# Optimization experiments

Measured on AMD Instinct MI355X. Metric: run time of the kernel, lower is better.

The kernel has to match this reference:

```python
import jax, jax.numpy as jnp
import numpy as np

VOCAB, ATTR, B = 50257, 16, 256
EMB, ATTR_EMB, HID, ZDIM = 300, 200, 700, 500
MAXLEN = 30
SOS_IDX, EOS_IDX = 1, 2


def setup_inputs() -> dict:
    ks = jax.random.split(jax.random.key(0), 8)
    s = 0.02
    return {
        "z": jax.random.normal(ks[0], (B, ZDIM), jnp.float32),
        "l": jax.random.randint(ks[1], (B,), 0, ATTR),
        "emb_w": jax.random.normal(ks[2], (VOCAB, EMB), jnp.float32) * s,
        "attr_w": jax.random.normal(ks[3], (ATTR, ATTR_EMB), jnp.float32) * s,
        "W_ih": jax.random.normal(ks[4], (3 * HID, EMB), jnp.float32) * s,
        "W_hh": jax.random.normal(ks[5], (3 * HID, HID), jnp.float32) * s,
        "b_ih": jnp.zeros((3 * HID,), jnp.float32),
        "b_hh": jnp.zeros((3 * HID,), jnp.float32),
        "out_w": jax.random.normal(ks[6], (VOCAB, HID), jnp.float32) * s,
        "out_b": jnp.zeros((VOCAB,), jnp.float32),
    }


def gru_cell(x, h, W_ih, W_hh, b_ih, b_hh):
    # PyTorch GRU cell: r,z,n gate ordering
    gi = x @ W_ih.T + b_ih          # (B, 3H)
    gh = h @ W_hh.T + b_hh          # (B, 3H)
    i_r, i_z, i_n = jnp.split(gi, 3, axis=-1)
    h_r, h_z, h_n = jnp.split(gh, 3, axis=-1)
    r = jax.nn.sigmoid(i_r + h_r)
    zg = jax.nn.sigmoid(i_z + h_z)
    n = jnp.tanh(i_n + r * h_n)
    return (1.0 - zg) * n + zg * h


def reference(z, l, emb_w, attr_w, W_ih, W_hh, b_ih, b_hh, out_w, out_b):
    # hidden init: cat([z (B,500), attr_emb(l) (B,200)]) -> (B,700)
    h0 = jnp.concatenate([z, attr_w[l]], axis=-1)
    tok0 = jnp.full((B,), SOS_IDX, jnp.int32)
    keys = jax.random.split(jax.random.key(42), MAXLEN)

    def step(carry, k):
        h, tok = carry
        x = emb_w[tok]                                   # (B,300)
        h = gru_cell(x, h, W_ih, W_hh, b_ih, b_hh)       # (B,700)
        logits = h @ out_w.T + out_b                     # (B,VOCAB)
        # multinomial(softmax(logits), 1).detach()
        nxt = jax.lax.stop_gradient(
            jax.random.categorical(k, logits).astype(jnp.int32))
        return (h, nxt), (h, nxt)

    (h_last, _), (hy_t, y_t) = jax.lax.scan(step, (h0, tok0), keys)
    # final forced-EOS step
    eos = jnp.full((B,), EOS_IDX, jnp.int32)
    h_final = gru_cell(emb_w[eos], h_last, W_ih, W_hh, b_ih, b_hh)
    hy = jnp.concatenate([jnp.transpose(hy_t, (1, 0, 2)), h_final[:, None, :]], axis=1)  # (B,MAXLEN+1,700)
    y = jnp.concatenate([jnp.transpose(y_t, (1, 0)), eos[:, None]], axis=1)              # (B,MAXLEN+1)
    return hy, y
```

## Files before the change

### kernel.cpp

```cpp
#include <hip/hip_runtime.h>
#include <stdint.h>

#define VOCAB 50257
#define B 256
#define EMB 300
#define HID 700
#define G3 2100
#define ZDIM 500
#define ATTR_EMBD 200
#define MAXLEN 30
#define SEQ 31
#define HY_ELEMS (B*SEQ*HID)
#define KP 704
#define NKT 22
#define KIH 320
#define VPAD 50304
#define NVT 393
#define MPAD 2112
#define SOS_IDX 1
#define EOS_IDX 2
#define CHUNK 4096
#define TILE_STRIDE ((size_t)NKT * 2 * CHUNK)
#define NIT5 1572
#define NBLK5 1576

typedef _Float16 half8 __attribute__((ext_vector_type(8)));
typedef _Float16 half4 __attribute__((ext_vector_type(4)));
typedef float f32x4 __attribute__((ext_vector_type(4)));

typedef const __attribute__((address_space(1))) void* gas1_t;
typedef __attribute__((address_space(3))) void* las3_t;
__device__ __forceinline__ void gload_lds16(const void* g, void* l) {
  __builtin_amdgcn_global_load_lds((gas1_t)g, (las3_t)l, 16, 0, 0);
}

__device__ __forceinline__ uint32_t rotl32(uint32_t x, int r) {
  return (x << r) | (x >> (32 - r));
}

__device__ __forceinline__ void threefry2x32(uint32_t k0, uint32_t k1,
                                             uint32_t x0, uint32_t x1,
                                             uint32_t& o0, uint32_t& o1) {
  const uint32_t ks2 = k0 ^ k1 ^ 0x1BD11BDAu;
  x0 += k0; x1 += k1;
#define TF_R4(a, b, c, d)                                     \
  x0 += x1; x1 = rotl32(x1, a); x1 ^= x0;                     \
  x0 += x1; x1 = rotl32(x1, b); x1 ^= x0;                     \
  x0 += x1; x1 = rotl32(x1, c); x1 ^= x0;                     \
  x0 += x1; x1 = rotl32(x1, d); x1 ^= x0;
  TF_R4(13, 15, 26, 6)  x0 += k1;  x1 += ks2 + 1u;
  TF_R4(17, 29, 16, 24) x0 += ks2; x1 += k0 + 2u;
  TF_R4(13, 15, 26, 6)  x0 += k0;  x1 += k1 + 3u;
  TF_R4(17, 29, 16, 24) x0 += k1;  x1 += ks2 + 4u;
  TF_R4(13, 15, 26, 6)  x0 += ks2; x1 += k0 + 5u;
#undef TF_R4
  o0 = x0; o1 = x1;
}

__device__ __forceinline__ unsigned long long gumbel_pack(float s, uint32_t key0,
                                                          uint32_t key1, int b, int v) {
  uint32_t j = (uint32_t)(b * VOCAB + v);
  uint32_t o0, o1;
  threefry2x32(key0, key1, 0u, j, o0, o1);
  uint32_t bits = o0 ^ o1;
  float f = __uint_as_float((bits >> 9) | 0x3f800000u) - 1.0f;
  float u = fmaxf(f, 1.17549435e-38f);
  float g = -__logf(-__logf(u));
  s += g;
  uint32_t us = __float_as_uint(s);
  us = (us & 0x80000000u) ? ~us : (us | 0x80000000u);
  return ((unsigned long long)us << 32) | (uint32_t)(~(uint32_t)v);
}

struct hl16 { _Float16 hi, lo; };
__device__ __forceinline__ hl16 split16(float val, float scale) {
  float s = val * scale;
  _Float16 h = (_Float16)s;
  hl16 r;
  r.hi = h;
  r.lo = (_Float16)(s - (float)h);
  return r;
}

__global__ void k_init(const float* __restrict__ z, const int* __restrict__ l,
                       const float* __restrict__ attr_w, const float* __restrict__ emb_w,
                       float* __restrict__ hbuf0, uint32_t* __restrict__ keys,
                       unsigned long long* __restrict__ slots,
                       int* __restrict__ tok, float* __restrict__ y_out,
                       _Float16* __restrict__ h_hi, _Float16* __restrict__ h_lo,
                       _Float16* __restrict__ ht,
                       _Float16* __restrict__ x0_hi, _Float16* __restrict__ x0_lo,
                       _Float16* __restrict__ xe_hi, _Float16* __restrict__ xe_lo,
                       int full) {
  int idx = blockIdx.x * blockDim.x + threadIdx.x;
  if (idx < B * HID) {
    int b = idx / HID, i = idx % HID;
    float v = (i < ZDIM) ? z[b * ZDIM + i]
                         : attr_w[l[b] * ATTR_EMBD + (i - ZDIM)];
    hbuf0[idx] = v;
    hl16 r = split16(v, 8.0f);
    h_hi[b * KP + i] = r.hi;
    h_lo[b * KP + i] = r.lo;
  }
  if (idx < MAXLEN) {
    uint32_t o0, o1;
    threefry2x32(0u, 42u, 0u, (uint32_t)idx, o0, o1);
    keys[2 * idx] = o0; keys[2 * idx + 1] = o1;
  }
  if (idx < MAXLEN * B) slots[idx] = 0ull;
  if (idx < B) {
    tok[idx] = SOS_IDX;
    tok[31 * B + idx] = EOS_IDX;
    y_out[idx * SEQ + MAXLEN] = 2.0f;
  }
  if (idx < B * 4) {
    int b = idx >> 2, k = HID + (idx & 3);
    h_hi[b * KP + k] = (_Float16)0.0f;
    h_lo[b * KP + k] = (_Float16)0.0f;
    int c = b >> 7, row = b & 127, e = k & 7;
    size_t tb = (size_t)c * TILE_STRIDE + (size_t)21 * 2 * CHUNK
              + (3 * 128 + row) * 8 + e;
    ht[tb] = (_Float16)0.0f;
    ht[tb + CHUNK] = (_Float16)0.0f;
  }
  if (full && idx < KIH) {
    float v0 = (idx < EMB) ? emb_w[SOS_IDX * EMB + idx] : 0.0f;
    float ve = (idx < EMB) ? emb_w[EOS_IDX * EMB + idx] : 0.0f;
    hl16 r0 = split16(v0, 8.0f);
    hl16 re = split16(ve, 8.0f);
    for (int b = 0; b < B; ++b) {
      x0_hi[b * KIH + idx] = r0.hi; x0_lo[b * KIH + idx] = r0.lo;
      xe_hi[b * KIH + idx] = re.hi; xe_lo[b * KIH + idx] = re.lo;
    }
  }
}

__global__ void k_wsplit(const float* __restrict__ out_w, _Float16* __restrict__ wt) {
  size_t idx = (size_t)blockIdx.x * blockDim.x + threadIdx.x;
  if (idx >= (size_t)NVT * NKT * 1024) return;
  int h4 = (int)(idx & 1023);
  int ktp = (int)(idx >> 10);
  int kt = ktp % NKT, p = ktp / NKT;
  int slot4 = h4 >> 1, e0 = (h4 & 1) * 4;
  int kc = slot4 >> 7, row = slot4 & 127;
  int v = p * 128 + row;
  int k = kt * 32 + kc * 8 + e0;
  float x[4];
  if (v < VOCAB && k + 3 < HID) {
    const float4 xv = *(const float4*)&out_w[(size_t)v * HID + k];
    x[0] = xv.x; x[1] = xv.y; x[2] = xv.z; x[3] = xv.w;
  } else {
#pragma unroll
    for (int j = 0; j < 4; ++j)
      x[j] = (v < VOCAB && k + j < HID) ? out_w[(size_t)v * HID + k + j] : 0.0f;
  }
  half4 hi, lo;
#pragma unroll
  for (int j = 0; j < 4; ++j) {
    hl16 r = split16(x[j], 64.0f);
    hi[j] = r.hi; lo[j] = r.lo;
  }
  size_t base = (size_t)p * TILE_STRIDE + (size_t)kt * 2 * CHUNK + slot4 * 8 + e0;
  *(half4*)&wt[base] = hi;
  *(half4*)&wt[base + CHUNK] = lo;
}

__global__ void k_gwsplit(const float* __restrict__ src, _Float16* __restrict__ hi,
                          _Float16* __restrict__ lo, int Msrc, int Ksrc, int Kpad,
                          int tot4) {
  int idx = blockIdx.x * blockDim.x + threadIdx.x;
  if (idx >= tot4) return;
  size_t i4 = (size_t)idx * 4;
  int m = (int)(i4 / Kpad), k = (int)(i4 % Kpad);
  half4 h, l;
#pragma unroll
  for (int j = 0; j < 4; ++j) {
    float x = (m < Msrc && k + j < Ksrc) ? src[(size_t)m * Ksrc + k + j] : 0.0f;
    hl16 r = split16(x, 64.0f);
    h[j] = r.hi; l[j] = r.lo;
  }
  *(half4*)&hi[i4] = h;
  *(half4*)&lo[i4] = l;
}

__global__ __launch_bounds__(256, 4)
void k_gates2(const _Float16* __restrict__ wih_hi, const _Float16* __restrict__ wih_lo,
              const _Float16* __restrict__ whh_hi, const _Float16* __restrict__ whh_lo,
              const _Float16* __restrict__ x_hi, const _Float16* __restrict__ x_lo,
              const _Float16* __restrict__ h_hi, const _Float16* __restrict__ h_lo,
              float* __restrict__ gi, float* __restrict__ gh) {
  const int zz = blockIdx.z;
  const _Float16* __restrict__ Whi = zz ? whh_hi : wih_hi;
  const _Float16* __restrict__ Wlo = zz ? whh_lo : wih_lo;
  const _Float16* __restrict__ Xhi = zz ? h_hi : x_hi;
  const _Float16* __restrict__ Xlo = zz ? h_lo : x_lo;
  const int Kz = zz ? KP : KIH;
  float* __restrict__ out = zz ? gh : gi;

  const int jbase = blockIdx.x * 64;
  const int bbase = blockIdx.y * 64;
  __shared__ float4 lds[2][4][256];
  const int tid = threadIdx.x, lane = tid & 63, wid = tid >> 6;
  const int wj = wid >> 1, wb2 = wid & 1;
  const size_t wrow = (size_t)(jbase + lane) * Kz;
  const size_t xrow = (size_t)(bbase + lane) * Kz;

  f32x4 acc[2][2];
#pragma unroll
  for (int i = 0; i < 2; ++i)
#pragma unroll
    for (int j = 0; j < 2; ++j) acc[i][j] = (f32x4)0.0f;

#define GSTAGE(bf, k0)                                                   \
  {                                                                      \
    gload_lds16(Whi + wrow + (k0) + wid * 8, &lds[bf][0][wid * 64]);     \
    gload_lds16(Wlo + wrow + (k0) + wid * 8, &lds[bf][1][wid * 64]);     \
    gload_lds16(Xhi + xrow + (k0) + wid * 8, &lds[bf][2][wid * 64]);     \
    gload_lds16(Xlo + xrow + (k0) + wid * 8, &lds[bf][3][wid * 64]);     \
  }

  const int nt = Kz / 32;
  GSTAGE(0, 0)
  for (int kt = 0; kt < nt; ++kt) {
    const int cur = kt & 1;
    __syncthreads();
    if (kt + 1 < nt) GSTAGE(cur ^ 1, (kt + 1) * 32)
    const int kcf = (lane >> 4) * 64 + (lane & 15);
    half8 a_hi[2], a_lo[2];
#pragma unroll
    for (int fv = 0; fv < 2; ++fv) {
      int s = kcf + wj * 32 + fv * 16;
      a_hi[fv] = *(const half8*)&lds[cur][0][s];
      a_lo[fv] = *(const half8*)&lds[cur][1][s];
    }
#pragma unroll
    for (int fb = 0; fb < 2; ++fb) {
      int s = kcf + wb2 * 32 + fb * 16;
      half8 b_hi = *(const half8*)&lds[cur][2][s];
      half8 b_lo = *(const half8*)&lds[cur][3][s];
#pragma unroll
      for (int fv = 0; fv < 2; ++fv) {
        acc[fv][fb] = __builtin_amdgcn_mfma_f32_16x16x32_f16(a_hi[fv], b_hi,
                                                             acc[fv][fb], 0, 0, 0);
        acc[fv][fb] = __builtin_amdgcn_mfma_f32_16x16x32_f16(a_hi[fv], b_lo,
                                                             acc[fv][fb], 0, 0, 0);
        acc[fv][fb] = __builtin_amdgcn_mfma_f32_16x16x32_f16(a_lo[fv], b_hi,
                                                             acc[fv][fb], 0, 0, 0);
      }
    }
  }
#undef GSTAGE

  const float c2 = 1.0f / 512.0f;
#pragma unroll
  for (int fb = 0; fb < 2; ++fb) {
    const int b = bbase + wb2 * 32 + fb * 16 + (lane & 15);
#pragma unroll
    for (int fv = 0; fv < 2; ++fv) {
#pragma unroll
      for (int r = 0; r < 4; ++r) {
        int j = jbase + wj * 32 + fv * 16 + (lane >> 4) * 4 + r;
        if (j < G3) out[b * G3 + j] = acc[fv][fb][r] * c2;
      }
    }
  }
}

__global__ void k_gates(const float* __restrict__ W_ih, const float* __restrict__ W_hh,
                        const float* __restrict__ emb_w, const float* __restrict__ hprev,
                        const int* __restrict__ tok,
                        float* __restrict__ gi, float* __restrict__ gh) {
  const int zz = blockIdx.z;
  const float* __restrict__ W = zz ? W_hh : W_ih;
  const int K = zz ? HID : EMB;
  float* __restrict__ out = zz ? gh : gi;
  __shared__ float w_lds[20][36];
  __shared__ float xh_lds[20][36];
  const int jbase = blockIdx.x * 32;
  const int bbase = blockIdx.y * 32;
  const int tid = threadIdx.x;
  const int tj = tid % 16, tb = tid / 16;
  float a00 = 0.f, a01 = 0.f, a10 = 0.f, a11 = 0.f;
  for (int k0 = 0; k0 < K; k0 += 20) {
    for (int idx = tid; idx < 640; idx += 256) {
      int col = idx / 20, kk = idx % 20;
      int j = jbase + col;
      w_lds[kk][col] = (j < G3) ? W[j * K + k0 + kk] : 0.0f;
      int b = bbase + col;
      float xv;
      if (zz) xv = hprev[b * HID + k0 + kk];
      else    xv = emb_w[tok[b] * EMB + k0 + kk];
      xh_lds[kk][col] = xv;
    }
    __syncthreads();
#pragma unroll
    for (int kk = 0; kk < 20; ++kk) {
      float w0 = w_lds[kk][tj * 2], w1 = w_lds[kk][tj * 2 + 1];
      float h0 = xh_lds[kk][tb * 2], h1 = xh_lds[kk][tb * 2 + 1];
      a00 += w0 * h0; a01 += w0 * h1;
      a10 += w1 * h0; a11 += w1 * h1;
    }
    __syncthreads();
  }
  int j0 = jbase + tj * 2, b0 = bbase + tb * 2;
  if (j0 < G3)     { out[b0 * G3 + j0] = a00;     out[(b0 + 1) * G3 + j0] = a01; }
  if (j0 + 1 < G3) { out[b0 * G3 + j0 + 1] = a10; out[(b0 + 1) * G3 + j0 + 1] = a11; }
}

__global__ void k_hnew(const float* __restrict__ gi, const float* __restrict__ gh,
                       const float* __restrict__ b_ih, const float* __restrict__ b_hh,
                       const float* __restrict__ hprev, float* __restrict__ hnext,
                       float* __restrict__ hy, _Float16* __restrict__ h_hi,
                       _Float16* __restrict__ h_lo, _Float16* __restrict__ ht, int t) {
  int idx = blockIdx.x * blockDim.x + threadIdx.x;
  if (idx >= B * HID) return;
  int b = idx / HID, i = idx % HID;
  float ir = gi[b * G3 + i]            + b_ih[i];
  float iz = gi[b * G3 + HID + i]      + b_ih[HID + i];
  float in_ = gi[b * G3 + 2 * HID + i] + b_ih[2 * HID + i];
  float hr = gh[b * G3 + i]            + b_hh[i];
  float hz = gh[b * G3 + HID + i]      + b_hh[HID + i];
  float hn = gh[b * G3 + 2 * HID + i]  + b_hh[2 * HID + i];
  float r  = 1.0f / (1.0f + expf(-(ir + hr)));
  float zg = 1.0f / (1.0f + expf(-(iz + hz)));
  float n  = tanhf(in_ + r * hn);
  float h  = (1.0f - zg) * n + zg * hprev[idx];
  hnext[idx] = h;
  hy[(size_t)b * SEQ * HID + (size_t)t * HID + i] = h;
  hl16 rr = split16(h, 8.0f);
  h_hi[b * KP + i] = rr.hi;
  h_lo[b * KP + i] = rr.lo;
  int c = b >> 7, row = b & 127;
  size_t tb = (size_t)c * TILE_STRIDE + (size_t)(i >> 5) * 2 * CHUNK
            + ((((i >> 3) & 3) * 128 + row) * 8) + (i & 7);
  ht[tb] = rr.hi;
  ht[tb + CHUNK] = rr.lo;
}

__global__ __launch_bounds__(256, 4)
void k_logits5(const _Float16* __restrict__ wt, const _Float16* __restrict__ ht,
               const float* __restrict__ out_b, const uint32_t* __restrict__ keys,
               unsigned long long* __restrict__ slot, int t) {
  const int item = (blockIdx.x & 7) * 197 + (blockIdx.x >> 3);
  if (item >= NIT5) return;
  const int p = item >> 2, vh = (item >> 1) & 1, c = item & 1;

  __shared__ float4 ldsh[2][1024];
  const int tid = threadIdx.x, lane = tid & 63, wid = tid >> 6;
  const int wv = wid >> 1, wb = wid & 1;
  const int lq = lane >> 4, lr = lane & 15;

  const _Float16* __restrict__ wp = wt + (size_t)p * TILE_STRIDE;
  const _Float16* __restrict__ hp = ht + (size_t)c * TILE_STRIDE;

  const int wslot = lq * 128 + vh * 64 + wv * 32 + lr;
  const int hslot = lq * 128 + wb * 64 + lr;

  f32x4 acc[2][4];
#pragma unroll
  for (int i = 0; i < 2; ++i)
#pragma unroll
    for (int j = 0; j < 4; ++j) acc[i][j] = (f32x4)0.0f;

  half8 wA[4], wB[4];

#define LOADW(W, ktv)                                                         \
  {                                                                           \
    const _Float16* bw = wp + (size_t)(ktv) * (2 * CHUNK);                    \
    _Pragma("unroll")                                                         \
    for (int fv = 0; fv < 2; ++fv) {                                          \
      W[fv * 2 + 0] = *(const half8*)(bw + (wslot + fv * 16) * 8);            \
      W[fv * 2 + 1] = *(const half8*)(bw + CHUNK + (wslot + fv * 16) * 8);    \
    }                                                                         \
  }
#define STAGEH(bf, ktv)                                                       \
  {                                                                           \
    const _Float16* bh = hp + (size_t)(ktv) * (2 * CHUNK);                    \
    _Pragma("unroll")                                                         \
    for (int j = 0; j < 4; ++j)                                               \
      gload_lds16(bh + (j * 256 + wid * 64 + lane) * 8,                       \
                  &ldsh[bf][j * 256 + wid * 64]);                             \
  }
#define COMPUTE(bf, W)                                                        \
  _Pragma("unroll")                                                           \
  for (int fb = 0; fb < 4; ++fb) {                                            \
    half8 hhi = *(const half8*)&ldsh[bf][hslot + fb * 16];                    \
    half8 hlo = *(const half8*)&ldsh[bf][512 + hslot + fb * 16];              \
    _Pragma("unroll")                                                         \
    for (int fv = 0; fv < 2; ++fv) {                                          \
      acc[fv][fb] = __builtin_amdgcn_mfma_f32_16x16x32_f16(                   \
          W[fv * 2 + 0], hhi, acc[fv][fb], 0, 0, 0);                          \
      acc[fv][fb] = __builtin_amdgcn_mfma_f32_16x16x32_f16(                   \
          W[fv * 2 + 0], hlo, acc[fv][fb], 0, 0, 0);                          \
      acc[fv][fb] = __builtin_amdgcn_mfma_f32_16x16x32_f16(                   \
          W[fv * 2 + 1], hhi, acc[fv][fb], 0, 0, 0);                          \
    }                                                                         \
  }

  LOADW(wA, 0)
  STAGEH(0, 0)
  __syncthreads();
#pragma unroll 1
  for (int kt = 0; kt < NKT; kt += 2) {
    if (kt + 1 < NKT) { STAGEH(1, kt + 1) LOADW(wB, kt + 1) }
    COMPUTE(0, wA)
    __syncthreads();
    if (kt + 2 < NKT) { STAGEH(0, kt + 2) LOADW(wA, kt + 2) }
    COMPUTE(1, wB)
    __syncthreads();
  }
#undef LOADW
#undef STAGEH
#undef COMPUTE

  const uint32_t key0 = keys[2 * t], key1 = keys[2 * t + 1];
  const float c2 = 1.0f / 512.0f;
  const int vbase0 = p * 128 + vh * 64 + wv * 32;
#pragma unroll
  for (int fb = 0; fb < 4; ++fb) {
    const int b = c * 128 + wb * 64 + fb * 16 + lr;
    unsigned long long best = 0ull;
#pragma unroll
    for (int fv = 0; fv < 2; ++fv) {
#pragma unroll
      for (int r = 0; r < 4; ++r) {
        int v = vbase0 + fv * 16 + lq * 4 + r;
        if (v < VOCAB) {
          float s = acc[fv][fb][r] * c2 + out_b[v];
          unsigned long long cand = gumbel_pack(s, key0, key1, b, v);
          if (cand > best) best = cand;
        }
      }
    }
    unsigned long long o;
    o = __shfl_xor(best, 16, 64); if (o > best) best = o;
    o = __shfl_xor(best, 32, 64); if (o > best) best = o;
    if (lq == 0) atomicMax(&slot[b], best);
  }
}

#define WPITCH 68
#define HPITCH 260
__global__ __launch_bounds__(256)
void k_logits_f32(const float* __restrict__ h, const float* __restrict__ out_w,
                  const float* __restrict__ out_b, const uint32_t* __restrict__ keys,
                  unsigned long long* __restrict__ slot, int t) {
  __shared__ float w_lds[20][WPITCH];
  __shared__ float h_lds[20][HPITCH];
  const int vbase = blockIdx.x * 64;
  const int tid = threadIdx.x;
  const int tv = tid % 8, tb = tid / 8;
  float acc[8][8];
#pragma unroll
  for (int i = 0; i < 8; ++i)
#pragma unroll
    for (int j = 0; j < 8; ++j) acc[i][j] = 0.f;

  for (int k0 = 0; k0 < HID; k0 += 20) {
    for (int idx = tid; idx < 64 * 20; idx += 256) {
      int vv = idx / 20, kk = idx % 20;
      int v = vbase + vv;
      w_lds[kk][vv] = (v < VOCAB) ? out_w[(size_t)v * HID + k0 + kk] : 0.0f;
    }
    for (int idx = tid; idx < 256 * 20; idx += 256) {
      int bb = idx / 20, kk = idx % 20;
      h_lds[kk][bb] = h[bb * HID + k0 + kk];
    }
    __syncthreads();
#pragma unroll
    for (int kk = 0; kk < 20; ++kk) {
      float wv[8], hv[8];
      *(float4*)&wv[0] = *(const float4*)&w_lds[kk][tv * 8];
      *(float4*)&wv[4] = *(const float4*)&w_lds[kk][tv * 8 + 4];
      *(float4*)&hv[0] = *(const float4*)&h_lds[kk][tb * 8];
      *(float4*)&hv[4] = *(const float4*)&h_lds[kk][tb * 8 + 4];
#pragma unroll
      for (int iv = 0; iv < 8; ++iv)
#pragma unroll
        for (int ib = 0; ib < 8; ++ib) acc[iv][ib] += wv[iv] * hv[ib];
    }
    __syncthreads();
  }

  const uint32_t key0 = keys[2 * t], key1 = keys[2 * t + 1];
#pragma unroll
  for (int ib = 0; ib < 8; ++ib) {
    const int b = tb * 8 + ib;
    unsigned long long best = 0ull;
#pragma unroll
    for (int iv = 0; iv < 8; ++iv) {
      int v = vbase + tv * 8 + iv;
      if (v >= VOCAB) continue;
      unsigned long long cand = gumbel_pack(acc[iv][ib] + out_b[v], key0, key1, b, v);
      if (cand > best) best = cand;
    }
#pragma unroll
    for (int off = 1; off < 8; off <<= 1) {
      unsigned long long other = __shfl_xor(best, off, 64);
      if (other > best) best = other;
    }
    if (tv == 0) atomicMax(&slot[b], best);
  }
}

__global__ void k_tok2(const unsigned long long* __restrict__ slot,
                       const float* __restrict__ emb_w,
                       int* __restrict__ tok_next, float* __restrict__ y_out,
                       _Float16* __restrict__ xc_hi, _Float16* __restrict__ xc_lo,
                       int t, int full) {
  const int b = blockIdx.x;
  const int c = threadIdx.x;
  unsigned long long p = slot[b];
  uint32_t v = ~((uint32_t)(p & 0xFFFFFFFFull));
  if (c == 0) {
    tok_next[b] = (int)v;
    y_out[b * SEQ + t] = (float)v;
  }
  if (!full) return;
  if (c < 75) {
    float4 xv = *(const float4*)&emb_w[(size_t)v * EMB + c * 4];
    half4 hi, lo;
    hl16 r0 = split16(xv.x, 8.0f); hi[0] = r0.hi; lo[0] = r0.lo;
    hl16 r1 = split16(xv.y, 8.0f); hi[1] = r1.hi; lo[1] = r1.lo;
    hl16 r2 = split16(xv.z, 8.0f); hi[2] = r2.hi; lo[2] = r2.lo;
    hl16 r3 = split16(xv.w, 8.0f); hi[3] = r3.hi; lo[3] = r3.lo;
    *(half4*)&xc_hi[b * KIH + c * 4] = hi;
    *(half4*)&xc_lo[b * KIH + c * 4] = lo;
  } else if (c < 80) {
    *(half4*)&xc_hi[b * KIH + c * 4] = (half4)(_Float16)0.0f;
    *(half4*)&xc_lo[b * KIH + c * 4] = (half4)(_Float16)0.0f;
  }
}

extern "C" void kernel_launch(void* const* d_in, const int* in_sizes, int n_in,
                              void* d_out, int out_size, void* d_ws, size_t ws_size,
                              hipStream_t stream) {
  const float* z      = (const float*)d_in[0];
  const int*   l      = (const int*)  d_in[1];
  const float* emb_w  = (const float*)d_in[2];
  const float* attr_w = (const float*)d_in[3];
  const float* W_ih   = (const float*)d_in[4];
  const float* W_hh   = (const float*)d_in[5];
  const float* b_ih   = (const float*)d_in[6];
  const float* b_hh   = (const float*)d_in[7];
  const float* out_w  = (const float*)d_in[8];
  const float* out_b  = (const float*)d_in[9];

  float* hy    = (float*)d_out;
  float* y_out = (float*)d_out + HY_ELEMS;

  char* ws = (char*)d_ws;
  size_t off = 0;
  uint32_t* keys            = (uint32_t*)(ws + off);           off += 256;
  unsigned long long* slots = (unsigned long long*)(ws + off); off += (size_t)MAXLEN * B * 8;
  int* tokbuf               = (int*)(ws + off);                off += (size_t)32 * B * 4;
  float* hbuf               = (float*)(ws + off);              off += (size_t)2 * B * HID * 4;
  float* gi                 = (float*)(ws + off);              off += (size_t)B * G3 * 4;
  float* gh                 = (float*)(ws + off);              off += (size_t)B * G3 * 4;
  _Float16* h_hi            = (_Float16*)(ws + off);           off += (size_t)B * KP * 2;
  _Float16* h_lo            = (_Float16*)(ws + off);           off += (size_t)B * KP * 2;
  _Float16* ht              = (_Float16*)(ws + off);           off += (size_t)2 * TILE_STRIDE * 2;
  _Float16* wt              = (_Float16*)(ws + off);           off += (size_t)NVT * TILE_STRIDE * 2;
  const size_t tier1_end = off;
  _Float16* wih_hi          = (_Float16*)(ws + off);           off += (size_t)MPAD * KIH * 2;
  _Float16* wih_lo          = (_Float16*)(ws + off);           off += (size_t)MPAD * KIH * 2;
  _Float16* whh_hi          = (_Float16*)(ws + off);           off += (size_t)MPAD * KP * 2;
  _Float16* whh_lo          = (_Float16*)(ws + off);           off += (size_t)MPAD * KP * 2;
  _Float16* x0_hi           = (_Float16*)(ws + off);           off += (size_t)B * KIH * 2;
  _Float16* x0_lo           = (_Float16*)(ws + off);           off += (size_t)B * KIH * 2;
  _Float16* xe_hi           = (_Float16*)(ws + off);           off += (size_t)B * KIH * 2;
  _Float16* xe_lo           = (_Float16*)(ws + off);           off += (size_t)B * KIH * 2;
  _Float16* xc_hi           = (_Float16*)(ws + off);           off += (size_t)B * KIH * 2;
  _Float16* xc_lo           = (_Float16*)(ws + off);           off += (size_t)B * KIH * 2;
  const size_t tier2_end = off;
  const int tier = (ws_size >= tier2_end) ? 2 : ((ws_size >= tier1_end) ? 1 : 0);

  k_init<<<(B * HID + 255) / 256, 256, 0, stream>>>(
      z, l, attr_w, emb_w, hbuf, keys, slots, tokbuf, y_out, h_hi, h_lo, ht,
      x0_hi, x0_lo, xe_hi, xe_lo, (tier == 2) ? 1 : 0);

  if (tier >= 1) {
    size_t tot = (size_t)NVT * NKT * 1024;
    k_wsplit<<<(int)((tot + 255) / 256), 256, 0, stream>>>(out_w, wt);
  }
  if (tier == 2) {
    int tih = MPAD * KIH / 4, thh = MPAD * KP / 4;
    k_gwsplit<<<(tih + 255) / 256, 256, 0, stream>>>(W_ih, wih_hi, wih_lo, G3, EMB, KIH, tih);
    k_gwsplit<<<(thh + 255) / 256, 256, 0, stream>>>(W_hh, whh_hi, whh_lo, G3, HID, KP, thh);
  }

  for (int t = 0; t <= MAXLEN; ++t) {
    float* hprev = hbuf + (t % 2) * B * HID;
    float* hnext = hbuf + ((t + 1) % 2) * B * HID;

    if (tier == 2) {
      const _Float16* xh = (t == 0) ? x0_hi : ((t == MAXLEN) ? xe_hi : xc_hi);
      const _Float16* xl = (t == 0) ? x0_lo : ((t == MAXLEN) ? xe_lo : xc_lo);
      dim3 g2(33, 4, 2);
      k_gates2<<<g2, 256, 0, stream>>>(wih_hi, wih_lo, whh_hi, whh_lo,
                                       xh, xl, h_hi, h_lo, gi, gh);
    } else {
      const int* tok_t = tokbuf + ((t == MAXLEN) ? 31 : t) * B;
      dim3 ggrid(66, 8, 2);
      k_gates<<<ggrid, 256, 0, stream>>>(W_ih, W_hh, emb_w, hprev, tok_t, gi, gh);
    }
    k_hnew<<<(B * HID + 255) / 256, 256, 0, stream>>>(gi, gh, b_ih, b_hh, hprev,
                                                      hnext, hy, h_hi, h_lo, ht, t);
    if (t < MAXLEN) {
      if (tier >= 1) {
        k_logits5<<<NBLK5, 256, 0, stream>>>(wt, ht, out_b, keys,
                                             slots + (size_t)t * B, t);
      } else {
        k_logits_f32<<<(VOCAB + 63) / 64, 256, 0, stream>>>(hnext, out_w, out_b, keys,
                                                            slots + (size_t)t * B, t);
      }
      k_tok2<<<B, 128, 0, stream>>>(slots + (size_t)t * B, emb_w,
                                    tokbuf + (t + 1) * B, y_out, xc_hi, xc_lo,
                                    t, (tier == 2) ? 1 : 0);
    }
  }
}
```

Before: 3.659 ms.

## Triple-buffer logits GEMM k-loop with one barrier per step and setprio

```diff
diff --git a/kernel.cpp b/kernel.cpp
--- a/kernel.cpp
+++ b/kernel.cpp
@@ -337,15 +337,15 @@
   ht[tb + CHUNK] = rr.lo;
 }
 
-__global__ __launch_bounds__(256, 4)
-void k_logits5(const _Float16* __restrict__ wt, const _Float16* __restrict__ ht,
+__global__ __launch_bounds__(256, 3)
+void k_logits7(const _Float16* __restrict__ wt, const _Float16* __restrict__ ht,
                const float* __restrict__ out_b, const uint32_t* __restrict__ keys,
                unsigned long long* __restrict__ slot, int t) {
   const int item = (blockIdx.x & 7) * 197 + (blockIdx.x >> 3);
   if (item >= NIT5) return;
   const int p = item >> 2, vh = (item >> 1) & 1, c = item & 1;
 
-  __shared__ float4 ldsh[2][1024];
+  __shared__ float4 ldsh[3][1024];
   const int tid = threadIdx.x, lane = tid & 63, wid = tid >> 6;
   const int wv = wid >> 1, wb = wid & 1;
   const int lq = lane >> 4, lr = lane & 15;
@@ -362,7 +362,7 @@
 #pragma unroll
     for (int j = 0; j < 4; ++j) acc[i][j] = (f32x4)0.0f;
 
-  half8 wA[4], wB[4];
+  half8 W0[4], W1[4], W2[4];
 
 #define LOADW(W, ktv)                                                         \
   {                                                                           \
@@ -381,11 +381,11 @@
       gload_lds16(bh + (j * 256 + wid * 64 + lane) * 8,                       \
                   &ldsh[bf][j * 256 + wid * 64]);                             \
   }
-#define COMPUTE(bf, W)                                                        \
+#define MFMAB(W, BF)                                                          \
   _Pragma("unroll")                                                           \
   for (int fb = 0; fb < 4; ++fb) {                                            \
-    half8 hhi = *(const half8*)&ldsh[bf][hslot + fb * 16];                    \
-    half8 hlo = *(const half8*)&ldsh[bf][512 + hslot + fb * 16];              \
+    half8 hhi = *(const half8*)&ldsh[BF][hslot + fb * 16];                    \
+    half8 hlo = *(const half8*)&ldsh[BF][512 + hslot + fb * 16];              \
     _Pragma("unroll")                                                         \
     for (int fv = 0; fv < 2; ++fv) {                                          \
       acc[fv][fb] = __builtin_amdgcn_mfma_f32_16x16x32_f16(                   \
@@ -396,22 +396,36 @@
           W[fv * 2 + 1], hhi, acc[fv][fb], 0, 0, 0);                          \
     }                                                                         \
   }
-
-  LOADW(wA, 0)
+#define STEP(ktv, BC, BP, WCUR, WNEW)                                         \
+  {                                                                           \
+    asm volatile("s_waitcnt vmcnt(4)" ::: "memory");                          \
+    __builtin_amdgcn_sched_barrier(0);                                        \
+    __builtin_amdgcn_s_barrier();                                             \
+    __builtin_amdgcn_sched_barrier(0);                                        \
+    if ((ktv) + 2 < NKT) {                                                    \
+      STAGEH(BP, (ktv) + 2)                                                   \
+      LOADW(WNEW, (ktv) + 2)                                                  \
+    }                                                                         \
+    __builtin_amdgcn_s_setprio(1);                                            \
+    MFMAB(WCUR, BC)                                                           \
+    __builtin_amdgcn_s_setprio(0);                                            \
+  }
+
   STAGEH(0, 0)
-  __syncthreads();
+  STAGEH(1, 1)
+  LOADW(W0, 0)
+  LOADW(W1, 1)
 #pragma unroll 1
-  for (int kt = 0; kt < NKT; kt += 2) {
-    if (kt + 1 < NKT) { STAGEH(1, kt + 1) LOADW(wB, kt + 1) }
-    COMPUTE(0, wA)
-    __syncthreads();
-    if (kt + 2 < NKT) { STAGEH(0, kt + 2) LOADW(wA, kt + 2) }
-    COMPUTE(1, wB)
-    __syncthreads();
-  }
+  for (int base = 0; base < 21; base += 3) {
+    STEP(base + 0, 0, 2, W0, W2)
+    STEP(base + 1, 1, 0, W1, W0)
+    STEP(base + 2, 2, 1, W2, W1)
+  }
+  STEP(21, 0, 2, W0, W2)
+#undef STEP
 #undef LOADW
 #undef STAGEH
-#undef COMPUTE
+#undef MFMAB
 
   const uint32_t key0 = keys[2 * t], key1 = keys[2 * t + 1];
   const float c2 = 1.0f / 512.0f;
@@ -608,7 +622,7 @@
                                                       hnext, hy, h_hi, h_lo, ht, t);
     if (t < MAXLEN) {
       if (tier >= 1) {
-        k_logits5<<<NBLK5, 256, 0, stream>>>(wt, ht, out_b, keys,
+        k_logits7<<<NBLK5, 256, 0, stream>>>(wt, ht, out_b, keys,
                                              slots + (size_t)t * B, t);
       } else {
         k_logits_f32<<<(VOCAB + 63) / 64, 256, 0, stream>>>(hnext, out_w, out_b, keys,
```

Result: slower. 3.739 ms (+2.2%).
